# Kernel tuning notes

Hardware: AMD Instinct MI355X
Metric: run time of the kernel (lower is better)

Reference implementation:

```python
import jax, jax.numpy as jnp
import numpy as np

N_ITER = 2
M = 0.0
AFF_SOFTMAX = 1.0
BIG = 1e16  # finite sentinel for invalid neighbors (CUDA kernel uses inf)


def _ssn(x, s):
    B, C, H, W = x.shape
    nh, nw = H // s, W // s
    S = nh * nw
    N = H * W
    # append_grid: concat (row, col) coordinate channels scaled by M/stoken
    ii, jj = jnp.meshgrid(jnp.arange(H), jnp.arange(W), indexing='ij')
    grid = jnp.stack([ii, jj], 0).astype(x.dtype) * (M / s)  # (2,H,W)
    xg = jnp.concatenate([x, jnp.broadcast_to(grid[None], (B, 2, H, W))], 1)
    C2 = C + 2
    # adaptive_avg_pool2d with exact divisibility == block mean
    cent = xg.reshape(B, C2, nh, s, nw, s).mean(axis=(3, 5)).reshape(B, C2, S)
    # nearest-neighbor init label map (exact divisibility => i//s)
    ly = jnp.broadcast_to((jnp.arange(H) // s)[:, None], (H, W)).reshape(-1)
    lx = jnp.broadcast_to((jnp.arange(W) // s)[None, :], (H, W)).reshape(-1)
    dy = jnp.repeat(jnp.arange(-1, 2), 3)  # 9-neighborhood offsets
    dx = jnp.tile(jnp.arange(-1, 2), 3)
    ny = ly[None, :] + dy[:, None]  # (9,N)
    nx = lx[None, :] + dx[:, None]
    valid = (ny >= 0) & (ny < nh) & (nx >= 0) & (nx < nw)
    nidx = jnp.clip(ny, 0, nh - 1) * nw + jnp.clip(nx, 0, nw - 1)  # (9,N)
    pix = jnp.arange(N)
    bidx = jnp.arange(B)[:, None, None]
    px = xg.reshape(B, C2, N)
    abs_aff = None
    for k in range(N_ITER):
        cg = cent[:, :, nidx]                              # (B,C2,9,N) gather
        dist = ((px[:, :, None, :] - cg) ** 2).sum(1)      # (B,9,N)
        dist = jnp.where(valid[None], dist, BIG)
        aff = jax.nn.softmax(-AFF_SOFTMAX * dist, axis=1)  # softmax over 9 nbrs
        aff = jnp.where(valid[None], aff, 0.0)
        # sparse_coo_tensor(...).to_dense() == scatter-add into (B,S,N)
        abs_aff = jnp.zeros((B, S, N), x.dtype).at[bidx, nidx[None], pix].add(aff)
        if k < N_ITER - 1:
            num = jnp.einsum('bsn,bcn->bcs', abs_aff, px)  # weighted bmm
            den = abs_aff.sum(2)[:, None] + 1e-16
            cent = num / den
    return abs_aff, S


def setup_inputs() -> dict:
    key = jax.random.key(0)
    x = jax.random.normal(key, (4, 32, 256, 256), dtype=jnp.float32)
    return {"x": x, "stoken_size": 16}


def reference(x, stoken_size):
    return _ssn(x, int(stoken_size))
```

## Files before the change

kernel.cpp:

```cpp
#include <hip/hip_runtime.h>

#define B_  4
#define C_  32
#define W_  256
#define N_  65536
#define NH_ 16
#define S_  256
#define PADP 260
#define PSTR 304

__device__ __forceinline__ float wave_sum(float v) {
    v += __shfl_down(v, 32);
    v += __shfl_down(v, 16);
    v += __shfl_down(v, 8);
    v += __shfl_down(v, 4);
    v += __shfl_down(v, 2);
    v += __shfl_down(v, 1);
    return v;
}

__device__ __forceinline__ void stage_tile(const float* __restrict__ x,
                                           int b, int sy, int sx, int t,
                                           float (*xsh)[PADP]) {
    const float* base = x + (size_t)b * C_ * N_ + (sy * 16) * W_ + sx * 16;
    #pragma unroll
    for (int i = 0; i < 8; ++i) {
        const int idx = i * 256 + t;
        const int c = idx >> 6, p4 = idx & 63;
        const float4 v = *(const float4*)(base + (size_t)c * N_ + (p4 >> 2) * W_ + (p4 & 3) * 4);
        *(float4*)&xsh[c][p4 * 4] = v;
    }
}

__device__ __forceinline__ void compute_aff(const float xv[C_], const float (*cl)[C_],
                                            int sy, int sx, float aff[9]) {
    float dist[9];
    #pragma unroll
    for (int k = 0; k < 9; ++k) {
        const int ny = sy + k / 3 - 1, nx = sx + k % 3 - 1;
        const bool valid = (ny >= 0) & (ny < NH_) & (nx >= 0) & (nx < NH_);
        float d = 0.f;
        #pragma unroll
        for (int c4 = 0; c4 < C_ / 4; ++c4) {
            const float4 cv = *(const float4*)&cl[k][c4 * 4];
            const float d0 = xv[c4 * 4 + 0] - cv.x;
            const float d1 = xv[c4 * 4 + 1] - cv.y;
            const float d2 = xv[c4 * 4 + 2] - cv.z;
            const float d3 = xv[c4 * 4 + 3] - cv.w;
            d += d0 * d0 + d1 * d1 + d2 * d2 + d3 * d3;
        }
        dist[k] = valid ? d : 1e30f;
    }
    float mind = dist[0];
    #pragma unroll
    for (int k = 1; k < 9; ++k) mind = fminf(mind, dist[k]);
    float sum = 0.f;
    #pragma unroll
    for (int k = 0; k < 9; ++k) {
        const float e = (dist[k] < 1e29f) ? __expf(mind - dist[k]) : 0.f;
        aff[k] = e;
        sum += e;
    }
    const float inv = 1.f / sum;
    #pragma unroll
    for (int k = 0; k < 9; ++k) aff[k] *= inv;
}

__global__ __launch_bounds__(256) void k_cent0(const float* __restrict__ x,
                                               float* __restrict__ cent0) {
    const int blk = blockIdx.x;
    const int b = blk >> 8, s = blk & 255;
    const int sy = s >> 4, sx = s & 15;
    const int t = threadIdx.x;
    const int w = t >> 6, lane = t & 63;
    const float* base = x + (size_t)b * C_ * N_ + (sy * 16) * W_ + sx * 16;
    #pragma unroll
    for (int i = 0; i < 8; ++i) {
        const int c = i * 4 + w;
        const float4 v = *(const float4*)(base + (size_t)c * N_ + (lane >> 2) * W_ + (lane & 3) * 4);
        const float sm = wave_sum(v.x + v.y + v.z + v.w);
        if (lane == 0) cent0[(size_t)blk * C_ + c] = sm * (1.0f / 256.0f);
    }
}

__global__ __launch_bounds__(256) void k_part(const float* __restrict__ x,
                                              const float* __restrict__ cent0,
                                              float* __restrict__ part,
                                              float* __restrict__ out) {
    const int blk = blockIdx.x;
    const int b = blk >> 8, s = blk & 255;
    const int sy = s >> 4, sx = s & 15;
    const int t = threadIdx.x;
    const int w = t >> 6, lane = t & 63;
    __shared__ float cl[9][C_];
    __shared__ float xsh[C_][PADP];
    __shared__ float affs[9][PADP];
    __shared__ float lden[4][9];
    {
        const int k = t >> 5, c = t & 31;
        const int ny = sy + k / 3 - 1, nx = sx + k % 3 - 1;
        const bool valid = (ny >= 0) & (ny < NH_) & (nx >= 0) & (nx < NH_);
        cl[k][c] = valid ? cent0[(size_t)(b * S_ + ny * NH_ + nx) * C_ + c] : 0.f;
    }
    if (t < 32) {
        const int ny = sy + 1, nx = sx + 1;
        const bool valid = (ny < NH_) & (nx < NH_);
        cl[8][t] = valid ? cent0[(size_t)(b * S_ + ny * NH_ + nx) * C_ + t] : 0.f;
    }
    stage_tile(x, b, sy, sx, t, xsh);
    {
        const float4 z = make_float4(0.f, 0.f, 0.f, 0.f);
        float4* plane = (float4*)out + ((size_t)blk << 14);
        #pragma unroll
        for (int i = 0; i < 32; ++i) {
            const int q = i * 256 + t;
            const int ty = q >> 10;
            const int tx = (q >> 2) & 15;
            if (((unsigned)(ty - sy + 1) > 2u) | ((unsigned)(tx - sx + 1) > 2u))
                plane[q] = z;
        }
    }
    __syncthreads();
    float xv[C_];
    #pragma unroll
    for (int c = 0; c < C_; ++c) xv[c] = xsh[c][t];
    float aff[9];
    compute_aff(xv, cl, sy, sx, aff);
    #pragma unroll
    for (int k = 0; k < 9; ++k) {
        affs[k][t] = aff[k];
        const float v = wave_sum(aff[k]);
        if (lane == 0) lden[w][k] = v;
    }
    __syncthreads();
    {
        const int k = t >> 5, c = t & 31;
        float acc = 0.f;
        #pragma unroll 4
        for (int p = 0; p < 256; p += 4) {
            const float4 a = *(const float4*)&affs[k][p];
            const float4 xc = *(const float4*)&xsh[c][p];
            acc += a.x * xc.x + a.y * xc.y + a.z * xc.z + a.w * xc.w;
        }
        part[(size_t)blk * PSTR + t] = acc;
    }
    if (t < 32) {
        float acc = 0.f;
        #pragma unroll 4
        for (int p = 0; p < 256; p += 4) {
            const float4 a = *(const float4*)&affs[8][p];
            const float4 xc = *(const float4*)&xsh[t][p];
            acc += a.x * xc.x + a.y * xc.y + a.z * xc.z + a.w * xc.w;
        }
        part[(size_t)blk * PSTR + 256 + t] = acc;
    }
    if (t < 9)
        part[(size_t)blk * PSTR + 288 + t] =
            lden[0][t] + lden[1][t] + lden[2][t] + lden[3][t];
}

__device__ __forceinline__ float gather_cent1(const float* __restrict__ part,
                                              int b, int ny, int nx, int c) {
    float num = 0.f, den = 0.f;
    #pragma unroll
    for (int k2 = 0; k2 < 9; ++k2) {
        const int syp = ny - (k2 / 3 - 1), sxp = nx - (k2 % 3 - 1);
        if ((syp >= 0) & (syp < NH_) & (sxp >= 0) & (sxp < NH_)) {
            const size_t base = (size_t)(b * S_ + syp * NH_ + sxp) * PSTR;
            num += part[base + k2 * 32 + c];
            den += part[base + 288 + k2];
        }
    }
    return num / (den + 1e-16f);
}

__global__ __launch_bounds__(256) void k_aff9(const float* __restrict__ x,
                                              const float* __restrict__ part,
                                              float* __restrict__ out) {
    const int blk = blockIdx.x;
    const int b = blk >> 8, s = blk & 255;
    const int sy = s >> 4, sx = s & 15;
    const int t = threadIdx.x;
    __shared__ float cl[9][C_];
    __shared__ float xsh[C_][PADP];
    __shared__ float affs[9][PADP];
    {
        const int k = t >> 5, c = t & 31;
        const int ny = sy + k / 3 - 1, nx = sx + k % 3 - 1;
        const bool valid = (ny >= 0) & (ny < NH_) & (nx >= 0) & (nx < NH_);
        cl[k][c] = valid ? gather_cent1(part, b, ny, nx, c) : 0.f;
    }
    if (t < 32) {
        const int ny = sy + 1, nx = sx + 1;
        const bool valid = (ny < NH_) & (nx < NH_);
        cl[8][t] = valid ? gather_cent1(part, b, ny, nx, t) : 0.f;
    }
    stage_tile(x, b, sy, sx, t, xsh);
    {
        const float4 z = make_float4(0.f, 0.f, 0.f, 0.f);
        float4* plane = (float4*)out + ((size_t)blk << 14);
        #pragma unroll
        for (int i = 32; i < 64; ++i) {
            const int q = i * 256 + t;
            const int ty = q >> 10;
            const int tx = (q >> 2) & 15;
            if (((unsigned)(ty - sy + 1) > 2u) | ((unsigned)(tx - sx + 1) > 2u))
                plane[q] = z;
        }
    }
    __syncthreads();
    float xv[C_];
    #pragma unroll
    for (int c = 0; c < C_; ++c) xv[c] = xsh[c][t];
    float aff[9];
    compute_aff(xv, cl, sy, sx, aff);
    #pragma unroll
    for (int k = 0; k < 9; ++k) affs[k][t] = aff[k];
    __syncthreads();
    #pragma unroll
    for (int i = 0; i < 3; ++i) {
        const int idx = i * 256 + t;
        if (idx < 576) {
            const int k = idx >> 6, j4 = idx & 63;
            const int ny = sy + k / 3 - 1, nx = sx + k % 3 - 1;
            if ((ny >= 0) & (ny < NH_) & (nx >= 0) & (nx < NH_)) {
                const float4 v = *(const float4*)&affs[k][j4 * 4];
                const int gq = (sy * 16 + (j4 >> 2)) * 64 + sx * 4 + (j4 & 3);
                ((float4*)out)[((size_t)(b * S_ + ny * NH_ + nx) << 14) + gq] = v;
            }
        }
    }
    if ((blk | t) == 0) out[(size_t)B_ * S_ * N_] = 256.0f;
}

extern "C" void kernel_launch(void* const* d_in, const int* in_sizes, int n_in,
                              void* d_out, int out_size, void* d_ws, size_t ws_size,
                              hipStream_t stream) {
    const float* x = (const float*)d_in[0];
    float* ws = (float*)d_ws;
    float* cent0 = ws;
    float* part  = ws + 32768;
    float* out   = (float*)d_out;

    hipLaunchKernelGGL(k_cent0, dim3(B_ * S_), dim3(256), 0, stream, x, cent0);
    hipLaunchKernelGGL(k_part,  dim3(B_ * S_), dim3(256), 0, stream, x, cent0, part, out);
    hipLaunchKernelGGL(k_aff9,  dim3(B_ * S_), dim3(256), 0, stream, x, part, out);
}
```

Measured before the change: 320.8 us.

## Use nontemporal stores and rebalance output zero-fill across kernels with staggered timing

Output writes, both zero-fill and affinity values, now use nontemporal vector stores so the large output stream can bypass cache retention. The zero-fill split between k_part and k_aff9 is rebalanced. k_part now zeroes the first 40 row-strips unconditionally, since k_aff9 overwrites the neighbour region afterwards. k_aff9 zeroes the remaining strips and still excludes the neighbour region. Even blocks zero before the first barrier and odd blocks after it, which staggers write traffic against compute and loads. The cost is a little extra redundant zeroing in k_part and a dropped unroll pragma on the zero loop.

```diff
diff --git a/kernel.cpp b/kernel.cpp
--- a/kernel.cpp
+++ b/kernel.cpp
@@ -9,6 +9,8 @@
 #define PADP 260
 #define PSTR 304
 
+typedef float vf4 __attribute__((ext_vector_type(4)));
+
 __device__ __forceinline__ float wave_sum(float v) {
     v += __shfl_down(v, 32);
     v += __shfl_down(v, 16);
@@ -18,6 +20,12 @@
     v += __shfl_down(v, 1);
     return v;
 }
+
+__device__ __forceinline__ void nt_store4(float* p, float a, float b, float c, float d) {
+    vf4 v = {a, b, c, d};
+    __builtin_nontemporal_store(v, (vf4*)p);
+}
+__device__ __forceinline__ void nt_zero4(float* p) { nt_store4(p, 0.f, 0.f, 0.f, 0.f); }
 
 __device__ __forceinline__ void stage_tile(const float* __restrict__ x,
                                            int b, int sy, int sx, int t,
@@ -83,6 +91,20 @@
     }
 }
 
+template <bool EXCL>
+__device__ __forceinline__ void zero_strip(float* plane, int t, int r0, int r1,
+                                           int sy, int sx) {
+    for (int i = r0; i < r1; ++i) {
+        const int q = i * 256 + t;
+        if (EXCL) {
+            const int ty = q >> 10, tx = (q >> 2) & 15;
+            if (((unsigned)(ty - sy + 1) <= 2u) & ((unsigned)(tx - sx + 1) <= 2u))
+                continue;
+        }
+        nt_zero4(plane + q * 4);
+    }
+}
+
 __global__ __launch_bounds__(256) void k_part(const float* __restrict__ x,
                                               const float* __restrict__ cent0,
                                               float* __restrict__ part,
@@ -92,6 +114,8 @@
     const int sy = s >> 4, sx = s & 15;
     const int t = threadIdx.x;
     const int w = t >> 6, lane = t & 63;
+    const bool early = (blk & 1) == 0;
+    float* plane = out + ((size_t)blk << 16);
     __shared__ float cl[9][C_];
     __shared__ float xsh[C_][PADP];
     __shared__ float affs[9][PADP];
@@ -108,18 +132,7 @@
         cl[8][t] = valid ? cent0[(size_t)(b * S_ + ny * NH_ + nx) * C_ + t] : 0.f;
     }
     stage_tile(x, b, sy, sx, t, xsh);
-    {
-        const float4 z = make_float4(0.f, 0.f, 0.f, 0.f);
-        float4* plane = (float4*)out + ((size_t)blk << 14);
-        #pragma unroll
-        for (int i = 0; i < 32; ++i) {
-            const int q = i * 256 + t;
-            const int ty = q >> 10;
-            const int tx = (q >> 2) & 15;
-            if (((unsigned)(ty - sy + 1) > 2u) | ((unsigned)(tx - sx + 1) > 2u))
-                plane[q] = z;
-        }
-    }
+    if (early) zero_strip<false>(plane, t, 0, 40, sy, sx);
     __syncthreads();
     float xv[C_];
     #pragma unroll
@@ -133,6 +146,7 @@
         if (lane == 0) lden[w][k] = v;
     }
     __syncthreads();
+    if (!early) zero_strip<false>(plane, t, 0, 40, sy, sx);
     {
         const int k = t >> 5, c = t & 31;
         float acc = 0.f;
@@ -181,6 +195,8 @@
     const int b = blk >> 8, s = blk & 255;
     const int sy = s >> 4, sx = s & 15;
     const int t = threadIdx.x;
+    const bool early = (blk & 1) == 0;
+    float* plane = out + ((size_t)blk << 16);
     __shared__ float cl[9][C_];
     __shared__ float xsh[C_][PADP];
     __shared__ float affs[9][PADP];
@@ -196,18 +212,7 @@
         cl[8][t] = valid ? gather_cent1(part, b, ny, nx, t) : 0.f;
     }
     stage_tile(x, b, sy, sx, t, xsh);
-    {
-        const float4 z = make_float4(0.f, 0.f, 0.f, 0.f);
-        float4* plane = (float4*)out + ((size_t)blk << 14);
-        #pragma unroll
-        for (int i = 32; i < 64; ++i) {
-            const int q = i * 256 + t;
-            const int ty = q >> 10;
-            const int tx = (q >> 2) & 15;
-            if (((unsigned)(ty - sy + 1) > 2u) | ((unsigned)(tx - sx + 1) > 2u))
-                plane[q] = z;
-        }
-    }
+    if (early) zero_strip<true>(plane, t, 40, 64, sy, sx);
     __syncthreads();
     float xv[C_];
     #pragma unroll
@@ -217,6 +222,7 @@
     #pragma unroll
     for (int k = 0; k < 9; ++k) affs[k][t] = aff[k];
     __syncthreads();
+    if (!early) zero_strip<true>(plane, t, 40, 64, sy, sx);
     #pragma unroll
     for (int i = 0; i < 3; ++i) {
         const int idx = i * 256 + t;
@@ -224,9 +230,10 @@
             const int k = idx >> 6, j4 = idx & 63;
             const int ny = sy + k / 3 - 1, nx = sx + k % 3 - 1;
             if ((ny >= 0) & (ny < NH_) & (nx >= 0) & (nx < NH_)) {
-                const float4 v = *(const float4*)&affs[k][j4 * 4];
                 const int gq = (sy * 16 + (j4 >> 2)) * 64 + sx * 4 + (j4 & 3);
-                ((float4*)out)[((size_t)(b * S_ + ny * NH_ + nx) << 14) + gq] = v;
+                float* dst = out + (((size_t)(b * S_ + ny * NH_ + nx) << 16) + gq * 4);
+                nt_store4(dst, affs[k][j4 * 4], affs[k][j4 * 4 + 1],
+                               affs[k][j4 * 4 + 2], affs[k][j4 * 4 + 3]);
             }
         }
     }
```

Result: no change. 317.4 us (-1.1%).
